# Optimization experiments

Hardware: AMD Instinct MI355X
Metric: run time of the kernel (lower is better)

The kernel has to match this reference:

```python
import jax, jax.numpy as jnp
import numpy as np

B, N, D = 4, 4096, 64
TAU_FLOW, TAU_COLOR, TAU_PROX = 0.8, 0.7, 0.5
GAMMA, ETA, NU = 5.0, 1.0, 1.0
SIGMA = 0.1  # default sigma in calculate_proximity_similarity


def setup_inputs() -> dict:
    key = jax.random.key(0)
    k1, k2, k3, k4 = jax.random.split(key, 4)
    flow = jax.random.normal(k1, (B, N, 3), dtype=jnp.float32)
    color = jax.random.uniform(k2, (B, N, 3), dtype=jnp.float32) * 255.0  # raw 0-255 colors
    coord = jax.random.normal(k3, (B, N, 3), dtype=jnp.float32)
    features = jax.random.normal(k4, (B, N, D), dtype=jnp.float32)
    return {"flow": flow, "color": color, "coord": coord, "features": features}


def _cdist(x):
    # batched pairwise euclidean distance: [B,N,d] -> [B,N,N]
    sq = jnp.sum(x * x, axis=-1)
    d2 = sq[:, :, None] + sq[:, None, :] - 2.0 * jnp.einsum('bnd,bmd->bnm', x, x)
    return jnp.sqrt(jnp.maximum(d2, 0.0))


def _contrast_loss(features, sim, tau):
    # within_sample_contrastive_loss + compute_contrastive_loss (score_higher_positive=True)
    fn = features / (jnp.linalg.norm(features, axis=-1, keepdims=True) + 1e-7)
    fs = jnp.einsum('bnd,bmd->bnm', fn, fn)  # feature cosine similarity [B,N,N]
    g_plus = jax.nn.sigmoid(GAMMA * (sim - tau))   # 1/(1+exp(gamma*(tau-s)))
    g_minus = jax.nn.sigmoid(GAMMA * (tau - sim))  # 1/(1+exp(gamma*(s-tau)))
    s_plus_exp = jnp.sum(jnp.exp(ETA * fs * g_plus), axis=-1)    # [B,N]
    s_minus_exp = jnp.sum(jnp.exp(-NU * fs * g_minus), axis=-1)  # [B,N]
    loss_per_point = jnp.log1p(s_plus_exp) / ETA + jnp.log1p(s_minus_exp) / NU
    # mean over points per sample, then mean over batch, negated
    return -jnp.mean(loss_per_point)


def reference(flow, color, coord, features):
    # flow cosine similarity
    fnorm = jnp.linalg.norm(flow, axis=-1)
    flow_sim = jnp.einsum('bnd,bmd->bnm', flow, flow) / (fnorm[:, :, None] * fnorm[:, None, :] + 1e-8)
    # color similarity: 1 - normalized cdist on colors/255
    c = color / 255.0
    color_sim = 1.0 - _cdist(c) / jnp.sqrt(jnp.float32(color.shape[-1]))
    # proximity similarity: exp(-d / (2*sigma^2))
    prox_sim = jnp.exp(-_cdist(coord) / (2.0 * SIGMA ** 2))
    loss = (1.0 * _contrast_loss(features, flow_sim, TAU_FLOW)
            + 1.0 * _contrast_loss(features, color_sim, TAU_COLOR)
            + 1.0 * _contrast_loss(features, prox_sim, TAU_PROX))
    return loss
```

## Files before the change

kernel.cpp:

```cpp
#include <hip/hip_runtime.h>
#include <math.h>

#define B_ 4
#define N_ 4096
#define BN_ (B_*N_)
#define NT 64
#define NCH 8

typedef __bf16 v8bf __attribute__((ext_vector_type(8)));
typedef unsigned short u16x8 __attribute__((ext_vector_type(8)));
typedef float v4f __attribute__((ext_vector_type(4)));

#define LOG2E 1.44269504088896340736f
#define CPROX (-50.0f*LOG2E)
#define INVSQRT3 0.57735026918962576f
#define GS (1.0f/1.4f)
#define GC_FLOW  (0.5f - 0.8f*GS)
#define GC_COLOR (0.5f - 0.7f*GS)
#define GC_PROX  (0.5f - 0.5f*GS)

__device__ __forceinline__ float fexp2(float x){ return __builtin_amdgcn_exp2f(x); }
__device__ __forceinline__ float fsqrt(float x){ return __builtin_amdgcn_sqrtf(x); }

extern "C" __global__ __launch_bounds__(256) void prep_k(
    const float* __restrict__ flow, const float* __restrict__ color,
    const float* __restrict__ coord, const float* __restrict__ feat,
    unsigned short* __restrict__ fn, float* __restrict__ scal)
{
  const int wave = blockIdx.x*4 + (threadIdx.x>>6);
  const int lane = threadIdx.x & 63;
  float v = feat[(size_t)wave*64 + lane];
  float ss = v*v;
  #pragma unroll
  for (int d=32; d; d>>=1) ss += __shfl_xor(ss, d);
  float sc = 1.0f/(sqrtf(ss)+1e-7f);
  float x = v*sc;
  unsigned u = __builtin_bit_cast(unsigned, x);
  unsigned r = (u + 0x7fffu + ((u>>16)&1u)) >> 16;
  fn[(size_t)wave*64+lane] = (unsigned short)r;
  if (lane==0) {
    float fx=flow[wave*3+0], fy=flow[wave*3+1], fz=flow[wave*3+2];
    float rn = 1.0f/sqrtf(fx*fx+fy*fy+fz*fz + 1e-8f);
    const float k = 1.0f/255.0f;
    float cx=color[wave*3+0]*k, cy=color[wave*3+1]*k, cz=color[wave*3+2]*k;
    float px=coord[wave*3+0], py=coord[wave*3+1], pz=coord[wave*3+2];
    float* o = scal + (size_t)wave*12;
    o[0]=fx*rn; o[1]=fy*rn; o[2]=fz*rn;
    o[3]=cx; o[4]=cy; o[5]=cz;
    o[6]=cx*cx+cy*cy+cz*cz;
    o[7]=px; o[8]=py; o[9]=pz;
    o[10]=px*px+py*py+pz*pz;
    o[11]=0.f;
  }
}

extern "C" __global__ __launch_bounds__(256,2) void main_k(
    const unsigned short* __restrict__ fn, const float* __restrict__ scal,
    float* __restrict__ part_row, float* __restrict__ part2)
{
  __shared__ unsigned short fnj[64*64];
  __shared__ float scj[64*12];
  __shared__ float colacc[4][64][6];

  const int ti = blockIdx.x & 63;
  const int k  = blockIdx.x >> 6;
  const int b  = blockIdx.y;
  const int nt = (k==7) ? 5 : 4;
  const int c0 = k*4;

  const int tid  = threadIdx.x;
  const int w    = tid >> 6;
  const int lane = tid & 63;
  const int g    = lane >> 4;
  const int col  = lane & 15;
  const int irow0 = ti*64 + w*16;

  const unsigned short* fnb = fn + (size_t)b*N_*64;
  const float* scb = scal + (size_t)b*N_*12;

  const int arow = irow0 + col;
  v8bf a0 = __builtin_bit_cast(v8bf, *(const u16x8*)(fnb + (size_t)arow*64 + g*8));
  v8bf a1 = __builtin_bit_cast(v8bf, *(const u16x8*)(fnb + (size_t)arow*64 + 32 + g*8));

  float fhi[4][3], ci[4][3], pi[4][3];
  #pragma unroll
  for (int r=0;r<4;++r) {
    const float* s = scb + (size_t)(irow0 + g*4 + r)*12;
    v4f s0 = *(const v4f*)(s), s1 = *(const v4f*)(s+4), s2 = *(const v4f*)(s+8);
    fhi[r][0]=s0.x; fhi[r][1]=s0.y; fhi[r][2]=s0.z;
    ci[r][0]=s0.w;  ci[r][1]=s1.x;  ci[r][2]=s1.y;
    pi[r][0]=s1.w;  pi[r][1]=s2.x;  pi[r][2]=s2.y;
  }

  float spa[3][4], sma[3][4];
  #pragma unroll
  for (int l=0;l<3;++l)
    #pragma unroll
    for (int r=0;r<4;++r){ spa[l][r]=0.f; sma[l][r]=0.f; }

  for (int tt=0; tt<nt; ++tt) {
    const int c  = c0 + tt;
    const int tj = (ti + c) & 63;
    const unsigned short* fng = fnb + (size_t)tj*64*64;
    const float* scg = scb + (size_t)tj*64*12;

    __syncthreads();
    #pragma unroll
    for (int q=0;q<2;++q) {
      int idx = tid + q*256;
      int row = idx>>3, seg = idx&7;
      const float4 src = *(const float4*)(fng + (size_t)row*64 + seg*8);
      *(float4*)((char*)fnj + row*128 + ((seg*16) ^ ((row&7)<<4))) = src;
    }
    if (tid < 192) {
      int row = tid/3, seg = tid - row*3;
      *(float4*)(scj + row*12 + seg*4) = *(const float4*)(scg + (size_t)row*12 + seg*4);
    }
    __syncthreads();

    #pragma unroll
    for (int sub=0; sub<4; ++sub) {
      const int jloc = sub*16 + col;
      const int sw = (jloc&7)<<4;
      const char* rowp = (const char*)fnj + jloc*128;
      v8bf b0 = __builtin_bit_cast(v8bf, *(const u16x8*)(rowp + ((g*16) ^ sw)));
      v8bf b1 = __builtin_bit_cast(v8bf, *(const u16x8*)(rowp + ((64 + g*16) ^ sw)));
      v4f j0 = *(const v4f*)(scj + jloc*12);
      v4f j1 = *(const v4f*)(scj + jloc*12 + 4);
      v4f j2 = *(const v4f*)(scj + jloc*12 + 8);

      v4f acc = {0.f,0.f,0.f,0.f};
      acc = __builtin_amdgcn_mfma_f32_16x16x32_bf16(a0, b0, acc, 0,0,0);
      acc = __builtin_amdgcn_mfma_f32_16x16x32_bf16(a1, b1, acc, 0,0,0);

      float cp0=0.f, cp1=0.f, cp2=0.f, cp3=0.f, cp4=0.f, cp5=0.f;

      #pragma unroll
      for (int r=0;r<4;++r) {
        const float fs = acc[r];
        const float sf = fhi[r][0]*j0.x + fhi[r][1]*j0.y + fhi[r][2]*j0.z;
        float dcx = ci[r][0]-j0.w, dcy = ci[r][1]-j1.x, dcz = ci[r][2]-j1.y;
        float d2c = fmaf(dcx,dcx, fmaf(dcy,dcy, dcz*dcz));
        const float scl = fmaf(fsqrt(d2c), -INVSQRT3, 1.0f);
        float dpx = pi[r][0]-j1.w, dpy = pi[r][1]-j2.x, dpz = pi[r][2]-j2.y;
        float d2p = fmaf(dpx,dpx, fmaf(dpy,dpy, dpz*dpz));
        const float spr = fexp2(fsqrt(d2p) * CPROX);
        const float fsl = fs * LOG2E;
        const float E2 = fexp2(-fsl);
        {
          float tt2 = __builtin_fminf(__builtin_fmaxf(fmaf(sf, GS, GC_FLOW), 0.f), 1.f);
          float gp = tt2*tt2*fmaf(tt2, -2.f, 3.f);
          float e1 = fexp2(fsl*gp);
          float e2 = E2*e1;
          spa[0][r] += e1; sma[0][r] += e2; cp0 += e1; cp1 += e2;
        }
        {
          float tt2 = __builtin_fminf(__builtin_fmaxf(fmaf(scl, GS, GC_COLOR), 0.f), 1.f);
          float gp = tt2*tt2*fmaf(tt2, -2.f, 3.f);
          float e1 = fexp2(fsl*gp);
          float e2 = E2*e1;
          spa[1][r] += e1; sma[1][r] += e2; cp2 += e1; cp3 += e2;
        }
        {
          float tt2 = __builtin_fminf(__builtin_fmaxf(fmaf(spr, GS, GC_PROX), 0.f), 1.f);
          float gp = tt2*tt2*fmaf(tt2, -2.f, 3.f);
          float e1 = fexp2(fsl*gp);
          float e2 = E2*e1;
          spa[2][r] += e1; sma[2][r] += e2; cp4 += e1; cp5 += e2;
        }
      }

      cp0 += __shfl_xor(cp0,16); cp0 += __shfl_xor(cp0,32);
      cp1 += __shfl_xor(cp1,16); cp1 += __shfl_xor(cp1,32);
      cp2 += __shfl_xor(cp2,16); cp2 += __shfl_xor(cp2,32);
      cp3 += __shfl_xor(cp3,16); cp3 += __shfl_xor(cp3,32);
      cp4 += __shfl_xor(cp4,16); cp4 += __shfl_xor(cp4,32);
      cp5 += __shfl_xor(cp5,16); cp5 += __shfl_xor(cp5,32);
      if (lane < 16) {
        float* ca = colacc[w][jloc];
        ca[0]=cp0; ca[1]=cp1; ca[2]=cp2; ca[3]=cp3; ca[4]=cp4; ca[5]=cp5;
      }
    }
    __syncthreads();
    if (c >= 1 && c <= 31) {
      for (int s = tid; s < 384; s += 256) {
        int jl = s/6, kk = s - 6*jl;
        float v = colacc[0][jl][kk]+colacc[1][jl][kk]+colacc[2][jl][kk]+colacc[3][jl][kk];
        part2[(((size_t)b*31 + (c-1))*N_ + tj*64 + jl)*6 + kk] = v;
      }
    }
  }

  #pragma unroll
  for (int l=0;l<3;++l)
    #pragma unroll
    for (int r=0;r<4;++r) {
      float a=spa[l][r], cc=sma[l][r];
      #pragma unroll
      for (int d=1; d<16; d<<=1){ a += __shfl_xor(a,d); cc += __shfl_xor(cc,d); }
      spa[l][r]=a; sma[l][r]=cc;
    }
  if (col==0) {
    #pragma unroll
    for (int r=0;r<4;++r) {
      float* o = part_row + (((size_t)b*NCH + k)*N_ + irow0 + g*4 + r)*6;
      o[0]=spa[0][r]; o[1]=sma[0][r];
      o[2]=spa[1][r]; o[3]=sma[1][r];
      o[4]=spa[2][r]; o[5]=sma[2][r];
    }
  }
}

extern "C" __global__ __launch_bounds__(256) void fin1_k(
    const float* __restrict__ part_row, const float* __restrict__ part2,
    float* __restrict__ partial)
{
  const int pt = blockIdx.x*256 + threadIdx.x;
  const int b = pt >> 12;
  const int i = pt & (N_-1);
  float s[6] = {0.f,0.f,0.f,0.f,0.f,0.f};
  #pragma unroll
  for (int kc=0;kc<NCH;++kc) {
    const float* pp = part_row + (((size_t)b*NCH + kc)*N_ + i)*6;
    #pragma unroll
    for (int q=0;q<6;++q) s[q] += pp[q];
  }
  for (int c=1;c<=31;++c) {
    const float* pp = part2 + (((size_t)b*31 + (c-1))*N_ + i)*6;
    #pragma unroll
    for (int q=0;q<6;++q) s[q] += pp[q];
  }
  float acc = log1pf(s[0]) + log1pf(s[1]) + log1pf(s[2])
            + log1pf(s[3]) + log1pf(s[4]) + log1pf(s[5]);
  #pragma unroll
  for (int d=32; d; d>>=1) acc += __shfl_xor(acc, d);
  __shared__ float wsum[4];
  if ((threadIdx.x&63)==0) wsum[threadIdx.x>>6] = acc;
  __syncthreads();
  if (threadIdx.x==0) partial[blockIdx.x] = wsum[0]+wsum[1]+wsum[2]+wsum[3];
}

extern "C" __global__ void fin2_k(const float* __restrict__ partial, float* __restrict__ out)
{
  float acc = partial[threadIdx.x];
  #pragma unroll
  for (int d=32; d; d>>=1) acc += __shfl_xor(acc, d);
  if (threadIdx.x==0) out[0] = -acc * (1.0f/(float)BN_);
}

extern "C" void kernel_launch(void* const* d_in, const int* in_sizes, int n_in,
                              void* d_out, int out_size, void* d_ws, size_t ws_size,
                              hipStream_t stream)
{
  const float* flow  = (const float*)d_in[0];
  const float* color = (const float*)d_in[1];
  const float* coord = (const float*)d_in[2];
  const float* feat  = (const float*)d_in[3];
  char* ws = (char*)d_ws;
  unsigned short* fn = (unsigned short*)ws;
  float* scal     = (float*)(ws + 2097152);
  float* part_row = (float*)(ws + 2883584);
  float* part2    = (float*)(ws + 6029312);
  float* partial  = (float*)(ws + 18219008);
  float* outp = (float*)d_out;
  hipLaunchKernelGGL(prep_k, dim3(BN_/4), dim3(256), 0, stream,
                     flow, color, coord, feat, fn, scal);
  hipLaunchKernelGGL(main_k, dim3(NT*NCH, B_), dim3(256), 0, stream,
                     fn, scal, part_row, part2);
  hipLaunchKernelGGL(fin1_k, dim3(BN_/256), dim3(256), 0, stream,
                     part_row, part2, partial);
  hipLaunchKernelGGL(fin2_k, dim3(1), dim3(64), 0, stream, partial, outp);
}
```

Before: 118.0 us.

## Double-buffer j-tiles in LDS and rebalance into 11 chunks of 3 tiles

The main kernel now stages the next j-tile's features and scalars through registers while computing the current tile, using two LDS buffers (including the column accumulators). This cuts one barrier per tile and hides global-load latency. The work split moves from 8 chunks of 4–5 tiles to 11 chunks of exactly 3 tiles, with launch bounds raised to 3 blocks per SM so more blocks are resident. Column shuffle reductions are skipped for tiles whose column sums are unused. The cost is doubled LDS use and more partial-row output for the finisher to read.

New measurement: 159.5 us. 1.35x slower.

```diff
diff --git a/kernel.cpp b/kernel.cpp
--- a/kernel.cpp
+++ b/kernel.cpp
@@ -5,7 +5,7 @@
 #define N_ 4096
 #define BN_ (B_*N_)
 #define NT 64
-#define NCH 8
+#define NCH 11
 
 typedef __bf16 v8bf __attribute__((ext_vector_type(8)));
 typedef unsigned short u16x8 __attribute__((ext_vector_type(8)));
@@ -54,19 +54,18 @@
   }
 }
 
-extern "C" __global__ __launch_bounds__(256,2) void main_k(
+extern "C" __global__ __launch_bounds__(256,3) void main_k(
     const unsigned short* __restrict__ fn, const float* __restrict__ scal,
     float* __restrict__ part_row, float* __restrict__ part2)
 {
-  __shared__ unsigned short fnj[64*64];
-  __shared__ float scj[64*12];
-  __shared__ float colacc[4][64][6];
+  __shared__ unsigned short fnj[2][64*64];
+  __shared__ float scj[2][64*12];
+  __shared__ float colacc[2][4][64][6];
 
   const int ti = blockIdx.x & 63;
   const int k  = blockIdx.x >> 6;
   const int b  = blockIdx.y;
-  const int nt = (k==7) ? 5 : 4;
-  const int c0 = k*4;
+  const int c0 = k*3;
 
   const int tid  = threadIdx.x;
   const int w    = tid >> 6;
@@ -78,6 +77,10 @@
   const unsigned short* fnb = fn + (size_t)b*N_*64;
   const float* scb = scal + (size_t)b*N_*12;
 
+  const int srow = tid>>3, sseg = tid&7;
+  const int ssw  = (srow&7)<<4;
+  const int scrow = tid/3, scseg = tid-3*(tid/3);
+
   const int arow = irow0 + col;
   v8bf a0 = __builtin_bit_cast(v8bf, *(const u16x8*)(fnb + (size_t)arow*64 + g*8));
   v8bf a1 = __builtin_bit_cast(v8bf, *(const u16x8*)(fnb + (size_t)arow*64 + 32 + g*8));
@@ -98,36 +101,57 @@
     #pragma unroll
     for (int r=0;r<4;++r){ spa[l][r]=0.f; sma[l][r]=0.f; }
 
-  for (int tt=0; tt<nt; ++tt) {
-    const int c  = c0 + tt;
+  {
+    const int tj = (ti + c0) & 63;
+    const unsigned short* fng = fnb + (size_t)tj*4096;
+    const float* scg = scb + (size_t)tj*768;
+    float4 f0 = *(const float4*)(fng + (size_t)srow*64 + sseg*8);
+    float4 f1 = *(const float4*)(fng + (size_t)(srow+32)*64 + sseg*8);
+    *(float4*)((char*)fnj[0] + srow*128 + ((sseg*16)^ssw)) = f0;
+    *(float4*)((char*)fnj[0] + (srow+32)*128 + ((sseg*16)^ssw)) = f1;
+    if (tid < 192)
+      *(float4*)(scj[0] + scrow*12 + scseg*4) = *(const float4*)(scg + (size_t)scrow*12 + scseg*4);
+  }
+  __syncthreads();
+
+  int cprev=-1, tjprev=0;
+  for (int t2=0; t2<3; ++t2) {
+    const int p  = t2&1;
+    const int c  = c0 + t2;
     const int tj = (ti + c) & 63;
-    const unsigned short* fng = fnb + (size_t)tj*64*64;
-    const float* scg = scb + (size_t)tj*64*12;
-
-    __syncthreads();
-    #pragma unroll
-    for (int q=0;q<2;++q) {
-      int idx = tid + q*256;
-      int row = idx>>3, seg = idx&7;
-      const float4 src = *(const float4*)(fng + (size_t)row*64 + seg*8);
-      *(float4*)((char*)fnj + row*128 + ((seg*16) ^ ((row&7)<<4))) = src;
-    }
-    if (tid < 192) {
-      int row = tid/3, seg = tid - row*3;
-      *(float4*)(scj + row*12 + seg*4) = *(const float4*)(scg + (size_t)row*12 + seg*4);
-    }
-    __syncthreads();
+    const bool docol = (c>=1 && c<=31);
+    const bool more  = (t2<2);
+
+    float4 f0, f1, sv;
+    if (more) {
+      const int tjn = (ti + c + 1) & 63;
+      const unsigned short* fng = fnb + (size_t)tjn*4096;
+      const float* scg = scb + (size_t)tjn*768;
+      f0 = *(const float4*)(fng + (size_t)srow*64 + sseg*8);
+      f1 = *(const float4*)(fng + (size_t)(srow+32)*64 + sseg*8);
+      if (tid < 192) sv = *(const float4*)(scg + (size_t)scrow*12 + scseg*4);
+    }
+
+    if (t2>0 && cprev>=1 && cprev<=31) {
+      const int pp = p^1;
+      for (int s=tid; s<384; s+=256) {
+        int jl=s/6, kk=s-6*jl;
+        float v = colacc[pp][0][jl][kk]+colacc[pp][1][jl][kk]
+                + colacc[pp][2][jl][kk]+colacc[pp][3][jl][kk];
+        part2[(((size_t)b*31 + (cprev-1))*N_ + tjprev*64 + jl)*6 + kk] = v;
+      }
+    }
 
     #pragma unroll
     for (int sub=0; sub<4; ++sub) {
       const int jloc = sub*16 + col;
       const int sw = (jloc&7)<<4;
-      const char* rowp = (const char*)fnj + jloc*128;
+      const char* rowp = (const char*)fnj[p] + jloc*128;
       v8bf b0 = __builtin_bit_cast(v8bf, *(const u16x8*)(rowp + ((g*16) ^ sw)));
       v8bf b1 = __builtin_bit_cast(v8bf, *(const u16x8*)(rowp + ((64 + g*16) ^ sw)));
-      v4f j0 = *(const v4f*)(scj + jloc*12);
-      v4f j1 = *(const v4f*)(scj + jloc*12 + 4);
-      v4f j2 = *(const v4f*)(scj + jloc*12 + 8);
+      v4f j0 = *(const v4f*)(scj[p] + jloc*12);
+      v4f j1 = *(const v4f*)(scj[p] + jloc*12 + 4);
+      v4f j2 = *(const v4f*)(scj[p] + jloc*12 + 8);
 
       v4f acc = {0.f,0.f,0.f,0.f};
       acc = __builtin_amdgcn_mfma_f32_16x16x32_bf16(a0, b0, acc, 0,0,0);
@@ -170,24 +194,37 @@
         }
       }
 
-      cp0 += __shfl_xor(cp0,16); cp0 += __shfl_xor(cp0,32);
-      cp1 += __shfl_xor(cp1,16); cp1 += __shfl_xor(cp1,32);
-      cp2 += __shfl_xor(cp2,16); cp2 += __shfl_xor(cp2,32);
-      cp3 += __shfl_xor(cp3,16); cp3 += __shfl_xor(cp3,32);
-      cp4 += __shfl_xor(cp4,16); cp4 += __shfl_xor(cp4,32);
-      cp5 += __shfl_xor(cp5,16); cp5 += __shfl_xor(cp5,32);
-      if (lane < 16) {
-        float* ca = colacc[w][jloc];
-        ca[0]=cp0; ca[1]=cp1; ca[2]=cp2; ca[3]=cp3; ca[4]=cp4; ca[5]=cp5;
+      if (docol) {
+        cp0 += __shfl_xor(cp0,16); cp0 += __shfl_xor(cp0,32);
+        cp1 += __shfl_xor(cp1,16); cp1 += __shfl_xor(cp1,32);
+        cp2 += __shfl_xor(cp2,16); cp2 += __shfl_xor(cp2,32);
+        cp3 += __shfl_xor(cp3,16); cp3 += __shfl_xor(cp3,32);
+        cp4 += __shfl_xor(cp4,16); cp4 += __shfl_xor(cp4,32);
+        cp5 += __shfl_xor(cp5,16); cp5 += __shfl_xor(cp5,32);
+        if (lane < 16) {
+          float* ca = colacc[p][w][jloc];
+          ca[0]=cp0; ca[1]=cp1; ca[2]=cp2; ca[3]=cp3; ca[4]=cp4; ca[5]=cp5;
+        }
       }
     }
+
+    if (more) {
+      const int nb = p^1;
+      *(float4*)((char*)fnj[nb] + srow*128 + ((sseg*16)^ssw)) = f0;
+      *(float4*)((char*)fnj[nb] + (srow+32)*128 + ((sseg*16)^ssw)) = f1;
+      if (tid < 192) *(float4*)(scj[nb] + scrow*12 + scseg*4) = sv;
+    }
+
     __syncthreads();
-    if (c >= 1 && c <= 31) {
-      for (int s = tid; s < 384; s += 256) {
-        int jl = s/6, kk = s - 6*jl;
-        float v = colacc[0][jl][kk]+colacc[1][jl][kk]+colacc[2][jl][kk]+colacc[3][jl][kk];
-        part2[(((size_t)b*31 + (c-1))*N_ + tj*64 + jl)*6 + kk] = v;
-      }
+    cprev=c; tjprev=tj;
+  }
+
+  if (cprev>=1 && cprev<=31) {
+    for (int s=tid; s<384; s+=256) {
+      int jl=s/6, kk=s-6*jl;
+      float v = colacc[0][0][jl][kk]+colacc[0][1][jl][kk]
+              + colacc[0][2][jl][kk]+colacc[0][3][jl][kk];
+      part2[(((size_t)b*31 + (cprev-1))*N_ + tjprev*64 + jl)*6 + kk] = v;
     }
   }
 
@@ -260,8 +297,8 @@
   unsigned short* fn = (unsigned short*)ws;
   float* scal     = (float*)(ws + 2097152);
   float* part_row = (float*)(ws + 2883584);
-  float* part2    = (float*)(ws + 6029312);
-  float* partial  = (float*)(ws + 18219008);
+  float* part2    = (float*)(ws + 7208960);
+  float* partial  = (float*)(ws + 19398656);
   float* outp = (float*)d_out;
   hipLaunchKernelGGL(prep_k, dim3(BN_/4), dim3(256), 0, stream,
                      flow, color, coord, feat, fn, scal);
```
